# Performance work log

Hardware: AMD Instinct MI355X
Metric: run time of the kernel (lower is better)

## Reference

```python
import jax, jax.numpy as jnp
import numpy as np

N_BLADES = 32  # Cl(4,1) has 2^5 = 32 basis blades


def _gp_sign_bitwise(a, b):
    """Sign of e_a * e_b in Cl(4,1) via bitwise swap counting (numpy, static)."""
    a = np.asarray(a, dtype=np.int64)
    b = np.asarray(b, dtype=np.int64)
    a, b = np.broadcast_arrays(a, b)
    swaps = np.zeros(a.shape, dtype=np.int64)
    for i in range(5):
        b_has_i = (b >> i) & 1
        mask_gt = (~((1 << (i + 1)) - 1)) & 31
        val = a & mask_gt
        pc = (val & 1) + ((val >> 1) & 1) + ((val >> 2) & 1) + ((val >> 3) & 1) + ((val >> 4) & 1)
        swaps += b_has_i * pc
    comm_sign = np.where(swaps % 2 == 0, 1.0, -1.0)
    metric_sign = np.where(((a & 16) & (b & 16)) > 0, -1.0, 1.0)
    return (comm_sign * metric_sign).astype(np.float32)


_M = np.arange(N_BLADES)
PERM = (_M[:, None] ^ _M[None, :]).astype(np.int32)        # PERM[k, m] = m ^ k
SIGNS = _gp_sign_bitwise(_M[None, :], PERM)                 # sign(m, m^k), [32, 32]
PERM_J = jnp.asarray(PERM)
SIGNS_J = jnp.asarray(SIGNS)


def setup_inputs() -> dict:
    key = jax.random.key(0)
    kx, kw = jax.random.split(key)
    B, In, Out = 1024, 256, 256
    x = jax.random.normal(kx, (B, In, N_BLADES), dtype=jnp.float32)
    std = 0.5 / (In * N_BLADES) ** 0.5
    weight = jax.random.normal(kw, (Out, In, N_BLADES), dtype=jnp.float32) * std
    return {"x": x, "weight": weight}


def reference(x, weight):
    # x: [B, In, 32], weight: [Out, In, 32]
    # out[b, o, k] = sum_{i, m} x[b, i, m^k] * sign(m, m^k) * w[o, i, m]
    x_g = x[..., PERM_J] * SIGNS_J                 # [B, In, 32(k), 32(m)]
    out = jnp.einsum('bikm,oim->bok', x_g, weight)  # [B, Out, 32]
    return out
```

## Files before the change

### kernel.cpp

```cpp
#include <hip/hip_runtime.h>

typedef __attribute__((ext_vector_type(8))) short bf16x8;
typedef __attribute__((ext_vector_type(16))) float f32x16;
typedef __attribute__((ext_vector_type(8))) unsigned short ushort8;

#define N_BLADES 32
#define B_DIM 1024
#define IN_DIM 256
#define OUT_DIM 256
#define K_DIM (IN_DIM * N_BLADES)
#define N_DIM (OUT_DIM * N_BLADES)


__device__ __forceinline__ unsigned short f2bf(float f) {
    unsigned int u = __float_as_uint(f);
    u = (u + 0x7fff + ((u >> 16) & 1)) >> 16;
    return (unsigned short)u;
}

__device__ __forceinline__ float gp_sign(int a, int b) {
    int swaps = 0;
#pragma unroll
    for (int i = 0; i < 5; ++i) {
        int mask = (~((1 << (i + 1)) - 1)) & 31;
        swaps += ((b >> i) & 1) * __popc(a & mask);
    }
    float s = (swaps & 1) ? -1.0f : 1.0f;
    if (a & b & 16) s = -s;
    return s;
}

__device__ __forceinline__ void gload_lds16(const void* g, void* l) {
    __builtin_amdgcn_global_load_lds(
        (const __attribute__((address_space(1))) unsigned int*)g,
        (__attribute__((address_space(3))) unsigned int*)l, 16, 0, 0);
}

#define FENCE() asm volatile("" ::: "memory")
#define BAR()    { FENCE(); __builtin_amdgcn_s_barrier(); FENCE(); }
#define SCHED0() __builtin_amdgcn_sched_barrier(0)
#define LGKM(n)  { asm volatile("s_waitcnt lgkmcnt(" #n ")" ::: "memory"); }
#define VMC(n)   { asm volatile("s_waitcnt vmcnt(" #n ")" ::: "memory"); }

__global__ __launch_bounds__(256) void cast_kernel(const float4* __restrict__ x,
                                                   unsigned short* __restrict__ xb) {
    int t = blockIdx.x * 256 + threadIdx.x;
    float4 a = x[t * 2];
    float4 b = x[t * 2 + 1];
    ushort8 pk;
    pk[0] = f2bf(a.x); pk[1] = f2bf(a.y); pk[2] = f2bf(a.z); pk[3] = f2bf(a.w);
    pk[4] = f2bf(b.x); pk[5] = f2bf(b.y); pk[6] = f2bf(b.z); pk[7] = f2bf(b.w);
    *(ushort8*)(xb + (size_t)t * 8) = pk;
}

__global__ __launch_bounds__(256) void cast_w_perm_kernel(const float* __restrict__ w,
                                                          unsigned short* __restrict__ wb2) {
    int t = blockIdx.x * 256 + threadIdx.x;
    int o31   = t & 31;
    int c16   = (t >> 5) & 7;
    int panel = (t >> 8) & 7;
    int kt    = t >> 11;
    int o  = panel * 32 + o31;
    int k0 = kt * 64 + c16 * 8;
    const float4* src = (const float4*)(w + (long)o * K_DIM + k0);
    float4 a = src[0], b = src[1];
    ushort8 pk;
    pk[0] = f2bf(a.x); pk[1] = f2bf(a.y); pk[2] = f2bf(a.z); pk[3] = f2bf(a.w);
    pk[4] = f2bf(b.x); pk[5] = f2bf(b.y); pk[6] = f2bf(b.z); pk[7] = f2bf(b.w);
    *(ushort8*)(wb2 + (size_t)t * 8) = pk;
}

__device__ __forceinline__ bf16x8 shuffle_sign(bf16x8 v, int jx,
                                               unsigned int m0, unsigned int m1,
                                               unsigned int m2, unsigned int m3) {
    union { bf16x8 v8; unsigned int w[4]; } a, b;
    a.v8 = v;
    int s = jx >> 1;
    unsigned int t0 = (s & 1) ? a.w[1] : a.w[0];
    unsigned int t1 = (s & 1) ? a.w[0] : a.w[1];
    unsigned int t2 = (s & 1) ? a.w[3] : a.w[2];
    unsigned int t3 = (s & 1) ? a.w[2] : a.w[3];
    unsigned int u0 = (s & 2) ? t2 : t0;
    unsigned int u1 = (s & 2) ? t3 : t1;
    unsigned int u2 = (s & 2) ? t0 : t2;
    unsigned int u3 = (s & 2) ? t1 : t3;
    if (jx & 1) {
        u0 = (u0 >> 16) | (u0 << 16);
        u1 = (u1 >> 16) | (u1 << 16);
        u2 = (u2 >> 16) | (u2 << 16);
        u3 = (u3 >> 16) | (u3 << 16);
    }
    b.w[0] = u0 ^ m0; b.w[1] = u1 ^ m1; b.w[2] = u2 ^ m2; b.w[3] = u3 ^ m3;
    return b.v8;
}


#define ROWB 16384

__global__ __launch_bounds__(512, 1) void gemm_ko32_kernel(const unsigned short* __restrict__ xb,
                                                           const unsigned short* __restrict__ wb2,
                                                           float* __restrict__ Cws) {
    __shared__ char lds[163840];

    const int tid  = threadIdx.x;
    const int lane = tid & 63;
    const int wid  = tid >> 6;
    const int wr   = wid >> 2;
    const int wc   = wid & 3;
    const int l31  = lane & 31;
    const int l5   = lane >> 5;

    const int  kblk = blockIdx.x;
    const long row0 = (long)blockIdx.y * 128;
    const int  jx   = kblk & 7;
    const int  kq   = (kblk >> 3) & 3;

    const int rA = tid >> 2;
    const int c0 = tid & 3;
    const char* aSrcK = (const char*)xb + (row0 + rA) * ROWB;
    const int aoffB = (c0 ^ kq) * 16;
    const int adst0 = (rA >> 5) * 4096 + c0 * 512 + (rA & 31) * 16;

    unsigned int mk0, mk1, mk2, mk3;
    {
        unsigned int mw[4];
#pragma unroll
        for (int w_ = 0; w_ < 4; ++w_) {
            unsigned int m_ = 0;
#pragma unroll
            for (int e2 = 0; e2 < 2; ++e2) {
                int m = 8 * c0 + 2 * w_ + e2;
                if (gp_sign(m, m ^ kblk) < 0.0f) m_ |= 0x8000u << (16 * e2);
            }
            mw[w_] = m_;
        }
        mk0 = mw[0]; mk1 = mw[1]; mk2 = mw[2]; mk3 = mw[3];
    }

    const int  tid16 = tid * 16;
    const char* bSrc = (const char*)wb2 + tid16;

    const int aL = (wr * 2) * 4096 + l5 * 512 + l31 * 16;
    const int bL = 32768 + (wc * 2) * 4096 + l5 * 512 + l31 * 16;

#define B_STAGE(br, tb) { \
    _Pragma("unroll") for (int n = 0; n < 4; ++n) \
        gload_lds16(bSrc + (tb) + n * 8192, \
                    lds + 32768 + (br) * 32768 + n * 8192 + tid16); }
#define A_LOAD_E(kpb) { \
    rAe0 = *(const bf16x8*)(aSrcK + (kpb) + aoffB); \
    rAe1 = *(const bf16x8*)(aSrcK + (kpb) + aoffB + 64); }
#define A_LOAD_O(kpb) { \
    rAo0 = *(const bf16x8*)(aSrcK + (kpb) + aoffB); \
    rAo1 = *(const bf16x8*)(aSrcK + (kpb) + aoffB + 64); }
#define A_WRITE_E(ab) { \
    bf16x8 s0_ = shuffle_sign(rAe0, jx, mk0, mk1, mk2, mk3); \
    bf16x8 s1_ = shuffle_sign(rAe1, jx, mk0, mk1, mk2, mk3); \
    *(bf16x8*)(lds + (ab) * 16384 + adst0) = s0_; \
    *(bf16x8*)(lds + (ab) * 16384 + adst0 + 2048) = s1_; }
#define A_WRITE_O(ab) { \
    bf16x8 s0_ = shuffle_sign(rAo0, jx, mk0, mk1, mk2, mk3); \
    bf16x8 s1_ = shuffle_sign(rAo1, jx, mk0, mk1, mk2, mk3); \
    *(bf16x8*)(lds + (ab) * 16384 + adst0) = s0_; \
    *(bf16x8*)(lds + (ab) * 16384 + adst0 + 2048) = s1_; }

#define READ_G0(ab, br) { \
    aG0[0][0] = *(const bf16x8*)(lds + (ab)*16384 + aL + 0*4096 + 0*1024); \
    aG0[0][1] = *(const bf16x8*)(lds + (ab)*16384 + aL + 0*4096 + 1*1024); \
    aG0[1][0] = *(const bf16x8*)(lds + (ab)*16384 + aL + 1*4096 + 0*1024); \
    aG0[1][1] = *(const bf16x8*)(lds + (ab)*16384 + aL + 1*4096 + 1*1024); \
    bG0[0][0] = *(const bf16x8*)(lds + (br)*32768 + bL + 0*4096 + 0*1024); \
    bG0[0][1] = *(const bf16x8*)(lds + (br)*32768 + bL + 0*4096 + 1*1024); \
    bG0[1][0] = *(const bf16x8*)(lds + (br)*32768 + bL + 1*4096 + 0*1024); \
    bG0[1][1] = *(const bf16x8*)(lds + (br)*32768 + bL + 1*4096 + 1*1024); }
#define READ_G1(ab, br) { \
    aG1[0][0] = *(const bf16x8*)(lds + (ab)*16384 + aL + 0*4096 + 2*1024); \
    aG1[0][1] = *(const bf16x8*)(lds + (ab)*16384 + aL + 0*4096 + 3*1024); \
    aG1[1][0] = *(const bf16x8*)(lds + (ab)*16384 + aL + 1*4096 + 2*1024); \
    aG1[1][1] = *(const bf16x8*)(lds + (ab)*16384 + aL + 1*4096 + 3*1024); \
    bG1[0][0] = *(const bf16x8*)(lds + (br)*32768 + bL + 0*4096 + 2*1024); \
    bG1[0][1] = *(const bf16x8*)(lds + (br)*32768 + bL + 0*4096 + 3*1024); \
    bG1[1][0] = *(const bf16x8*)(lds + (br)*32768 + bL + 1*4096 + 2*1024); \
    bG1[1][1] = *(const bf16x8*)(lds + (br)*32768 + bL + 1*4096 + 3*1024); }
#define MFG0() \
    _Pragma("unroll") for (int s = 0; s < 2; ++s) \
    _Pragma("unroll") for (int mt = 0; mt < 2; ++mt) \
    _Pragma("unroll") for (int nt = 0; nt < 2; ++nt) \
        acc[mt][nt] = __builtin_amdgcn_mfma_f32_32x32x16_bf16(aG0[mt][s], bG0[nt][s], acc[mt][nt], 0, 0, 0);
#define MFG1() \
    _Pragma("unroll") for (int s = 0; s < 2; ++s) \
    _Pragma("unroll") for (int mt = 0; mt < 2; ++mt) \
    _Pragma("unroll") for (int nt = 0; nt < 2; ++nt) \
        acc[mt][nt] = __builtin_amdgcn_mfma_f32_32x32x16_bf16(aG1[mt][s], bG1[nt][s], acc[mt][nt], 0, 0, 0);

    f32x16 acc[2][2];
#pragma unroll
    for (int mt = 0; mt < 2; ++mt)
#pragma unroll
        for (int nt = 0; nt < 2; ++nt) acc[mt][nt] = (f32x16)0.0f;

    bf16x8 rAe0, rAe1, rAo0, rAo1;
    bf16x8 aG0[2][2], bG0[2][2], aG1[2][2], bG1[2][2];

    A_LOAD_E(0);
    SCHED0();
    B_STAGE(0, 0);
    B_STAGE(1, 32768);
    SCHED0();
    VMC(8);
    A_WRITE_E(0);
    SCHED0();
    A_LOAD_O(128);
    SCHED0();
    B_STAGE(2, 65536);
    SCHED0();
    VMC(6);
    LGKM(0);
    BAR();

#define TILE32(AB, ABN, BR, BRS, ALOAD, AWRITE, Texp) { \
    const int T_ = (Texp); \
    const int  kAr = ((T_ + 2) & 127) << 7; \
    const long kBg = (long)((T_ + 3) & 127) << 15; \
    READ_G0(AB, BR); \
    SCHED0(); \
    READ_G1(AB, BR); \
    SCHED0(); \
    ALOAD(kAr);             \
    SCHED0(); \
    B_STAGE(BRS, kBg);      \
    SCHED0(); \
    LGKM(8); MFG0(); \
    VMC(10);                \
    AWRITE(ABN); \
    SCHED0(); \
    LGKM(2); MFG1(); \
    LGKM(0); \
    VMC(6);                 \
    BAR(); }

    for (int t = 0; t < 32; ++t) {
        const int T4 = t * 4;
        TILE32(0, 1, 0, 3, A_LOAD_E, A_WRITE_O, T4);
        TILE32(1, 0, 1, 0, A_LOAD_O, A_WRITE_E, T4 + 1);
        TILE32(0, 1, 2, 1, A_LOAD_E, A_WRITE_O, T4 + 2);
        TILE32(1, 0, 3, 2, A_LOAD_O, A_WRITE_E, T4 + 3);
    }

#pragma unroll
    for (int mt = 0; mt < 2; ++mt)
#pragma unroll
        for (int nt = 0; nt < 2; ++nt) {
            long c = (long)kblk * 256 + wc * 64 + nt * 32 + l31;
#pragma unroll
            for (int r = 0; r < 16; ++r) {
                int  rl = (r & 3) + 8 * (r >> 2) + 4 * l5;
                long rb = row0 + wr * 64 + mt * 32 + rl;
                Cws[rb * N_DIM + c] = acc[mt][nt][r];
            }
        }

#undef B_STAGE
#undef A_LOAD_E
#undef A_LOAD_O
#undef A_WRITE_E
#undef A_WRITE_O
#undef READ_G0
#undef READ_G1
#undef MFG0
#undef MFG1
#undef TILE32
}

__global__ __launch_bounds__(256) void transpose_kernel(const float* __restrict__ Cws,
                                                        float* __restrict__ out) {
    __shared__ float t[32 * 260];
    const int tid = threadIdx.x;
    const long b  = blockIdx.x;
    const float4* src = (const float4*)(Cws + b * N_DIM);
    float4*       dst = (float4*)(out + b * N_DIM);
#pragma unroll
    for (int r = 0; r < 8; ++r) {
        int f = tid + r * 256;
        float4 v = src[f];
        int k  = f >> 6;
        int c4 = (f & 63) * 4;
        *(float4*)&t[k * 260 + c4] = v;
    }
    __syncthreads();
#pragma unroll
    for (int r = 0; r < 8; ++r) {
        int g  = tid + r * 256;
        int o  = g >> 3;
        int k0 = (g & 7) * 4;
        float4 v;
        v.x = t[(k0 + 0) * 260 + o];
        v.y = t[(k0 + 1) * 260 + o];
        v.z = t[(k0 + 2) * 260 + o];
        v.w = t[(k0 + 3) * 260 + o];
        dst[g] = v;
    }
}

__global__ __launch_bounds__(256) void fallback_gp_kernel(const float* __restrict__ x,
                                                          const float* __restrict__ w,
                                                          float* __restrict__ out) {
    __shared__ float xs[IN_DIM * 32];
    __shared__ float tab[1024];
    int tid = threadIdx.x;
    for (int idx = tid; idx < 1024; idx += 256) {
        int m = idx >> 5, k = idx & 31;
        tab[idx] = gp_sign(m, m ^ k);
    }
    int b = blockIdx.x;
    const float4* xrow = (const float4*)(x + (long)b * K_DIM);
    float4* xs4 = (float4*)xs;
    for (int idx = tid; idx < 2048; idx += 256) xs4[idx] = xrow[idx];
    __syncthreads();

    int wid = tid >> 6, lane = tid & 63;
    int o = blockIdx.y * 8 + wid;
    int k = lane & 31, half = lane >> 5;
    float acc = 0.f;
    const float* wrow = w + (long)o * K_DIM + half * 4096;
    for (int i = 0; i < 128; ++i) {
        int ib = (half * 128 + i) * 32;
#pragma unroll
        for (int m = 0; m < 32; ++m) {
            acc += xs[ib + (m ^ k)] * tab[m * 32 + k] * wrow[i * 32 + m];
        }
    }
    acc += __shfl_down(acc, 32);
    if (half == 0) out[((long)b * OUT_DIM + o) * 32 + k] = acc;
}

extern "C" void kernel_launch(void* const* d_in, const int* in_sizes, int n_in,
                              void* d_out, int out_size, void* d_ws, size_t ws_size,
                              hipStream_t stream) {
    const float* x = (const float*)d_in[0];
    const float* w = (const float*)d_in[1];
    float* out = (float*)d_out;

    const size_t xb_bytes  = (size_t)B_DIM * K_DIM * 2;
    const size_t wb_bytes  = (size_t)OUT_DIM * IN_DIM * 32 * 2;
    const size_t cw_bytes  = (size_t)B_DIM * N_DIM * 4;
    const size_t need = xb_bytes + wb_bytes + cw_bytes;

    if (ws_size >= need) {
        unsigned short* xbp = (unsigned short*)d_ws;
        unsigned short* wbp = (unsigned short*)((char*)d_ws + xb_bytes);
        float*          cws = (float*)((char*)d_ws + xb_bytes + wb_bytes);

        cast_kernel<<<dim3(4096), dim3(256), 0, stream>>>((const float4*)x, xbp);
        cast_w_perm_kernel<<<dim3(1024), dim3(256), 0, stream>>>(w, wbp);
        gemm_ko32_kernel<<<dim3(32, 8), dim3(512), 0, stream>>>(xbp, wbp, cws);
        transpose_kernel<<<dim3(B_DIM), dim3(256), 0, stream>>>(cws, out);
    } else {
        fallback_gp_kernel<<<dim3(B_DIM, OUT_DIM / 8), dim3(256), 0, stream>>>(x, w, out);
    }
}
```

Measured before the change: 176.5 us.

## XOR-swizzle A tile LDS layout and move A writes to tile start

Applies an XOR swizzle to the LDS row index of the A tile, keyed on the k-chunk, on both the shuffled writes and the MFMA fragment reads, to reduce LDS bank conflicts. It also moves the sign-shuffled A write for the next buffer to the start of each tile, ahead of the fragment reads. The vmcnt waits change to match, so the A global loads now have to land earlier, which may add stalls. The barrier count per tile is unchanged, but the prologue order of B staging and the A write is rearranged.

```diff
diff --git a/kernel.cpp b/kernel.cpp
--- a/kernel.cpp
+++ b/kernel.cpp
@@ -119,7 +119,7 @@
     const int c0 = tid & 3;
     const char* aSrcK = (const char*)xb + (row0 + rA) * ROWB;
     const int aoffB = (c0 ^ kq) * 16;
-    const int adst0 = (rA >> 5) * 4096 + c0 * 512 + (rA & 31) * 16;
+    const int adst0 = (rA >> 5) * 4096 + c0 * 512 + (((rA & 31) ^ (c0 << 1)) * 16);
 
     unsigned int mk0, mk1, mk2, mk3;
     {
@@ -140,8 +140,16 @@
     const int  tid16 = tid * 16;
     const char* bSrc = (const char*)wb2 + tid16;
 
-    const int aL = (wr * 2) * 4096 + l5 * 512 + l31 * 16;
-    const int bL = 32768 + (wc * 2) * 4096 + l5 * 512 + l31 * 16;
+    const int aLp = wr * 8192;
+    const int bLp = 32768 + wc * 8192;
+    const int aC0 = (0 + l5) * 512 + ((l31 ^ (((0 + l5) & 3) << 1)) * 16);
+    const int aC1 = (2 + l5) * 512 + ((l31 ^ (((2 + l5) & 3) << 1)) * 16);
+    const int aC2 = (4 + l5) * 512 + ((l31 ^ (((4 + l5) & 3) << 1)) * 16);
+    const int aC3 = (6 + l5) * 512 + ((l31 ^ (((6 + l5) & 3) << 1)) * 16);
+    const int bC0 = (0 + l5) * 512 + l31 * 16;
+    const int bC1 = (2 + l5) * 512 + l31 * 16;
+    const int bC2 = (4 + l5) * 512 + l31 * 16;
+    const int bC3 = (6 + l5) * 512 + l31 * 16;
 
 #define B_STAGE(br, tb) { \
     _Pragma("unroll") for (int n = 0; n < 4; ++n) \
@@ -165,23 +173,23 @@
     *(bf16x8*)(lds + (ab) * 16384 + adst0 + 2048) = s1_; }
 
 #define READ_G0(ab, br) { \
-    aG0[0][0] = *(const bf16x8*)(lds + (ab)*16384 + aL + 0*4096 + 0*1024); \
-    aG0[0][1] = *(const bf16x8*)(lds + (ab)*16384 + aL + 0*4096 + 1*1024); \
-    aG0[1][0] = *(const bf16x8*)(lds + (ab)*16384 + aL + 1*4096 + 0*1024); \
-    aG0[1][1] = *(const bf16x8*)(lds + (ab)*16384 + aL + 1*4096 + 1*1024); \
-    bG0[0][0] = *(const bf16x8*)(lds + (br)*32768 + bL + 0*4096 + 0*1024); \
-    bG0[0][1] = *(const bf16x8*)(lds + (br)*32768 + bL + 0*4096 + 1*1024); \
-    bG0[1][0] = *(const bf16x8*)(lds + (br)*32768 + bL + 1*4096 + 0*1024); \
-    bG0[1][1] = *(const bf16x8*)(lds + (br)*32768 + bL + 1*4096 + 1*1024); }
+    aG0[0][0] = *(const bf16x8*)(lds + (ab)*16384 + aLp + 0*4096 + aC0); \
+    aG0[0][1] = *(const bf16x8*)(lds + (ab)*16384 + aLp + 0*4096 + aC1); \
+    aG0[1][0] = *(const bf16x8*)(lds + (ab)*16384 + aLp + 1*4096 + aC0); \
+    aG0[1][1] = *(const bf16x8*)(lds + (ab)*16384 + aLp + 1*4096 + aC1); \
+    bG0[0][0] = *(const bf16x8*)(lds + (br)*32768 + bLp + 0*4096 + bC0); \
+    bG0[0][1] = *(const bf16x8*)(lds + (br)*32768 + bLp + 0*4096 + bC1); \
+    bG0[1][0] = *(const bf16x8*)(lds + (br)*32768 + bLp + 1*4096 + bC0); \
+    bG0[1][1] = *(const bf16x8*)(lds + (br)*32768 + bLp + 1*4096 + bC1); }
 #define READ_G1(ab, br) { \
-    aG1[0][0] = *(const bf16x8*)(lds + (ab)*16384 + aL + 0*4096 + 2*1024); \
-    aG1[0][1] = *(const bf16x8*)(lds + (ab)*16384 + aL + 0*4096 + 3*1024); \
-    aG1[1][0] = *(const bf16x8*)(lds + (ab)*16384 + aL + 1*4096 + 2*1024); \
-    aG1[1][1] = *(const bf16x8*)(lds + (ab)*16384 + aL + 1*4096 + 3*1024); \
-    bG1[0][0] = *(const bf16x8*)(lds + (br)*32768 + bL + 0*4096 + 2*1024); \
-    bG1[0][1] = *(const bf16x8*)(lds + (br)*32768 + bL + 0*4096 + 3*1024); \
-    bG1[1][0] = *(const bf16x8*)(lds + (br)*32768 + bL + 1*4096 + 2*1024); \
-    bG1[1][1] = *(const bf16x8*)(lds + (br)*32768 + bL + 1*4096 + 3*1024); }
+    aG1[0][0] = *(const bf16x8*)(lds + (ab)*16384 + aLp + 0*4096 + aC2); \
+    aG1[0][1] = *(const bf16x8*)(lds + (ab)*16384 + aLp + 0*4096 + aC3); \
+    aG1[1][0] = *(const bf16x8*)(lds + (ab)*16384 + aLp + 1*4096 + aC2); \
+    aG1[1][1] = *(const bf16x8*)(lds + (ab)*16384 + aLp + 1*4096 + aC3); \
+    bG1[0][0] = *(const bf16x8*)(lds + (br)*32768 + bLp + 0*4096 + bC2); \
+    bG1[0][1] = *(const bf16x8*)(lds + (br)*32768 + bLp + 0*4096 + bC3); \
+    bG1[1][0] = *(const bf16x8*)(lds + (br)*32768 + bLp + 1*4096 + bC2); \
+    bG1[1][1] = *(const bf16x8*)(lds + (br)*32768 + bLp + 1*4096 + bC3); }
 #define MFG0() \
     _Pragma("unroll") for (int s = 0; s < 2; ++s) \
     _Pragma("unroll") for (int mt = 0; mt < 2; ++mt) \
@@ -205,16 +213,17 @@
     A_LOAD_E(0);
     SCHED0();
     B_STAGE(0, 0);
+    SCHED0();
+    VMC(4);
+    A_WRITE_E(0);
+    SCHED0();
     B_STAGE(1, 32768);
     SCHED0();
-    VMC(8);
-    A_WRITE_E(0);
-    SCHED0();
     A_LOAD_O(128);
     SCHED0();
     B_STAGE(2, 65536);
     SCHED0();
-    VMC(6);
+    VMC(10);
     LGKM(0);
     BAR();
 
@@ -222,6 +231,9 @@
     const int T_ = (Texp); \
     const int  kAr = ((T_ + 2) & 127) << 7; \
     const long kBg = (long)((T_ + 3) & 127) << 15; \
+    VMC(4);                 \
+    AWRITE(ABN); \
+    SCHED0(); \
     READ_G0(AB, BR); \
     SCHED0(); \
     READ_G1(AB, BR); \
@@ -231,12 +243,7 @@
     B_STAGE(BRS, kBg);      \
     SCHED0(); \
     LGKM(8); MFG0(); \
-    VMC(10);                \
-    AWRITE(ABN); \
-    SCHED0(); \
-    LGKM(2); MFG1(); \
-    LGKM(0); \
-    VMC(6);                 \
+    LGKM(0); MFG1(); \
     BAR(); }
 
     for (int t = 0; t < 32; ++t) {
```

After: 162.2 us. -8.1%, faster.
